# Kernel optimization log

Measured on AMD Instinct MI355X. Metric: run time of the kernel, lower is better.

## Reference

```python
import jax, jax.numpy as jnp
import numpy as np

N_NODES = 50000


def gin_conv(x, src, dst, W, b, eps=0.0):
    # GINConv: nn((1+eps)*x_i + sum_{j in N(i)} x_j)
    agg = jax.ops.segment_sum(x[src], dst, num_segments=N_NODES)  # [N, D]
    h = (1.0 + eps) * x + agg
    return h @ W + b


def setup_inputs() -> dict:
    key = jax.random.key(0)
    ks = jax.random.split(key, 8)
    n, e = N_NODES, 800000
    d_in, d_h, d_out = 128, 128, 64
    feature = jax.random.normal(ks[0], (n, d_in), dtype=jnp.float32)
    edge_index = jax.random.randint(ks[1], (2, e), 0, n, dtype=jnp.int64)
    s1 = 1.0 / np.sqrt(d_in)
    sh = 1.0 / np.sqrt(d_h)
    W1 = jax.random.normal(ks[2], (d_in, d_h), dtype=jnp.float32) * s1
    b1 = jnp.zeros((d_h,), dtype=jnp.float32)
    Wh = jax.random.normal(ks[3], (d_h, d_h), dtype=jnp.float32) * sh
    bh = jnp.zeros((d_h,), dtype=jnp.float32)
    Wo = jax.random.normal(ks[4], (d_h, d_out), dtype=jnp.float32) * sh
    bo = jnp.zeros((d_out,), dtype=jnp.float32)
    return {"feature": feature, "edge_index": edge_index, "W1": W1, "b1": b1,
            "Wh": Wh, "bh": bh, "Wo": Wo, "bo": bo}


def reference(feature, edge_index, W1, b1, Wh, bh, Wo, bo):
    src, dst = edge_index[0], edge_index[1]
    x = gin_conv(feature, src, dst, W1, b1)
    x = jax.nn.relu(x)
    # one hidden layer (layer_num=3); dropout disabled (eval)
    x = gin_conv(x, src, dst, Wh, bh)
    x = jax.nn.relu(x)
    x = gin_conv(x, src, dst, Wo, bo)
    return jax.nn.log_softmax(x, axis=1)
```

## Files before the change

kernel.cpp:

```cpp
#include <hip/hip_runtime.h>

typedef short short8 __attribute__((ext_vector_type(8)));
typedef float f32x4 __attribute__((ext_vector_type(4)));


__device__ inline unsigned short f2bf(float f) {
    union { float f; unsigned u; } v; v.f = f;
    unsigned r = v.u + 0x7fffu + ((v.u >> 16) & 1u);
    return (unsigned short)(r >> 16);
}
__device__ inline unsigned pack2(float a, float b) {
    return (unsigned)f2bf(a) | ((unsigned)f2bf(b) << 16);
}
__device__ inline float bflo(unsigned u) { union { unsigned q; float f; } c; c.q = u << 16; return c.f; }
__device__ inline float bfhi(unsigned u) { union { unsigned q; float f; } c; c.q = u & 0xffff0000u; return c.f; }

#define ACC8(vv)                                     \
    acc[0] += bflo(vv.x); acc[1] += bfhi(vv.x);      \
    acc[2] += bflo(vv.y); acc[3] += bfhi(vv.y);      \
    acc[4] += bflo(vv.z); acc[5] += bfhi(vv.z);      \
    acc[6] += bflo(vv.w); acc[7] += bfhi(vv.w);

template <int TPN, typename F>
__device__ __forceinline__ void gather_acc(float acc[8], const uint4* __restrict__ x,
                                           int lane, int beg, int end, F geti) {
    int k = beg;
    for (; k + 8 <= end; k += 8) {
        int idx[8];
#pragma unroll
        for (int j = 0; j < 8; j++) idx[j] = geti(k + j);
        uint4 v[8];
#pragma unroll
        for (int j = 0; j < 8; j++) v[j] = x[(size_t)idx[j] * TPN + lane];
#pragma unroll
        for (int j = 0; j < 8; j++) { ACC8(v[j]) }
    }
    for (; k + 4 <= end; k += 4) {
        int i0 = geti(k), i1 = geti(k + 1), i2 = geti(k + 2), i3 = geti(k + 3);
        uint4 v0 = x[(size_t)i0 * TPN + lane];
        uint4 v1 = x[(size_t)i1 * TPN + lane];
        uint4 v2 = x[(size_t)i2 * TPN + lane];
        uint4 v3 = x[(size_t)i3 * TPN + lane];
        ACC8(v0) ACC8(v1) ACC8(v2) ACC8(v3)
    }
    for (; k < end; ++k) {
        uint4 v0 = x[(size_t)geti(k) * TPN + lane];
        ACC8(v0)
    }
}


#define EPB 2048
#define NE 8
#define BSH 9
#define MAXBKT 128
#define DCAP 10240

__global__ __launch_bounds__(256) void mega1(const int* __restrict__ dst, int* __restrict__ cnt2d,
                                             int e, int nbkt, int nblk,
                                             const float4* __restrict__ feat, uint2* __restrict__ featb,
                                             int cvtb, int nf4,
                                             const float* __restrict__ W1, const float* __restrict__ Wh,
                                             const float* __restrict__ Wo,
                                             unsigned short* __restrict__ W1t, unsigned short* __restrict__ Wht,
                                             unsigned short* __restrict__ Wot) {
    __shared__ int hist[MAXBKT];
    int t = threadIdx.x, b = blockIdx.x;
    if (b < nblk) {
        for (int j = t; j < nbkt; j += 256) hist[j] = 0;
        __syncthreads();
        int base = b * EPB;
#pragma unroll
        for (int j = 0; j < NE; j++) {
            int idx = base + t + 256 * j;
            if (idx < e) atomicAdd(&hist[dst[idx] >> BSH], 1);
        }
        __syncthreads();
        for (int j = t; j < nbkt; j += 256) cnt2d[j * nblk + b] = hist[j];
    } else if (b < nblk + cvtb) {
        int i = (b - nblk) * 256 + t;
        if (i < nf4) {
            float4 v = feat[i];
            featb[i] = make_uint2(pack2(v.x, v.y), pack2(v.z, v.w));
        }
    } else {
        int i = (b - nblk - cvtb) * 256 + t;
        if (i < 16384) {
            int k = i >> 7, nn = i & 127;
            W1t[nn * 128 + k] = f2bf(W1[i]);
        } else if (i < 32768) {
            int j = i - 16384, k = j >> 7, nn = j & 127;
            Wht[nn * 128 + k] = f2bf(Wh[j]);
        } else if (i < 40960) {
            int j = i - 32768, k = j >> 6, nn = j & 63;
            Wot[nn * 128 + k] = f2bf(Wo[j]);
        }
    }
}

__global__ __launch_bounds__(512) void scanB1(int* __restrict__ cnt2d, int* __restrict__ totals, int nblk) {
    __shared__ int s[512];
    int t = threadIdx.x, b = blockIdx.x;
    int v = (t < nblk) ? cnt2d[b * nblk + t] : 0;
    s[t] = v;
    __syncthreads();
    for (int off = 1; off < 512; off <<= 1) {
        int u = (t >= off) ? s[t - off] : 0;
        __syncthreads();
        s[t] += u;
        __syncthreads();
    }
    if (t < nblk) cnt2d[b * nblk + t] = s[t] - v;
    if (t == nblk - 1) totals[b] = s[t];
}

__global__ __launch_bounds__(128) void scanB2(const int* __restrict__ totals, int* __restrict__ bbase,
                                              int* __restrict__ row_ptr, int nbkt, int n, int e) {
    __shared__ int s[128];
    int t = threadIdx.x;
    int v = (t < nbkt) ? totals[t] : 0;
    s[t] = v;
    __syncthreads();
    for (int off = 1; off < 128; off <<= 1) {
        int u = (t >= off) ? s[t - off] : 0;
        __syncthreads();
        s[t] += u;
        __syncthreads();
    }
    if (t < nbkt) bbase[t] = s[t] - v;
    if (t == 0) row_ptr[n] = e;
}

__global__ __launch_bounds__(256) void binC(const int* __restrict__ src, const int* __restrict__ dst,
                                            const int* __restrict__ cnt2d, const int* __restrict__ bbase,
                                            unsigned* __restrict__ pairs, int e, int nbkt, int nblk) {
    __shared__ int hist[MAXBKT], loff[MAXBKT], cur[MAXBKT], gb[MAXBKT];
    __shared__ int sc[256];
    __shared__ unsigned sorted[EPB];
    int t = threadIdx.x, blk = blockIdx.x;
    for (int b = t; b < nbkt; b += 256) hist[b] = 0;
    __syncthreads();
    int base = blk * EPB;
    int cnt = min(EPB, e - base);
    unsigned packed[NE];
    int bb[NE];
#pragma unroll
    for (int j = 0; j < NE; j++) {
        int idx = base + t + 256 * j;
        bb[j] = -1;
        if (idx < e) {
            unsigned s0 = (unsigned)src[idx], d = (unsigned)dst[idx];
            int b = (int)(d >> BSH);
            bb[j] = b;
            packed[j] = s0 | ((d & ((1u << BSH) - 1)) << 16) | ((unsigned)b << 25);
            atomicAdd(&hist[b], 1);
        }
    }
    __syncthreads();
    int v = (t < nbkt) ? hist[t] : 0;
    sc[t] = v;
    __syncthreads();
    for (int off = 1; off < 256; off <<= 1) {
        int u = (t >= off) ? sc[t - off] : 0;
        __syncthreads();
        sc[t] += u;
        __syncthreads();
    }
    if (t < nbkt) {
        int ex = sc[t] - v;
        loff[t] = ex;
        cur[t] = ex;
        gb[t] = bbase[t] + cnt2d[t * nblk + blk];
    }
    __syncthreads();
#pragma unroll
    for (int j = 0; j < NE; j++) {
        if (bb[j] >= 0) {
            int r = atomicAdd(&cur[bb[j]], 1);
            sorted[r] = packed[j];
        }
    }
    __syncthreads();
    for (int i = t; i < cnt; i += 256) {
        unsigned w = sorted[i];
        int b = (int)(w >> 25);
        pairs[gb[b] + (i - loff[b])] = w;
    }
}

__global__ __launch_bounds__(512) void buildD(const unsigned* __restrict__ pairs,
                                              const int* __restrict__ totals, const int* __restrict__ bbase,
                                              int* __restrict__ row_ptr, unsigned short* __restrict__ csr, int n) {
    __shared__ int hist[512], off[512];
    __shared__ unsigned short lcsr[DCAP];
    int t = threadIdx.x, b = blockIdx.x;
    int cnt = totals[b], base = bbase[b];
    hist[t] = 0;
    __syncthreads();
    for (int i = t; i < cnt; i += 512)
        atomicAdd(&hist[(pairs[base + i] >> 16) & 511], 1);
    __syncthreads();
    int v = hist[t];
    off[t] = v;
    __syncthreads();
    for (int o = 1; o < 512; o <<= 1) {
        int u = (t >= o) ? off[t - o] : 0;
        __syncthreads();
        off[t] += u;
        __syncthreads();
    }
    int excl = off[t] - v;
    int node = (b << BSH) + t;
    if (node < n) row_ptr[node] = base + excl;
    __syncthreads();
    hist[t] = excl;
    __syncthreads();
    for (int i = t; i < cnt; i += 512) {
        unsigned w = pairs[base + i];
        int r = atomicAdd(&hist[(w >> 16) & 511], 1);
        if (r < DCAP) lcsr[r] = (unsigned short)(w & 0xFFFFu);
    }
    __syncthreads();
    int lim = min(cnt, DCAP);
    for (int i = t; i < lim; i += 512) csr[base + i] = lcsr[i];
}


#define ECAP 1024

template <bool SECOND>
__global__ __launch_bounds__(256) void fused_layer(
    const uint4* __restrict__ x, const int* __restrict__ row_ptr,
    const unsigned short* __restrict__ csr,
    const short8* __restrict__ Bt, const float* __restrict__ bias,
    unsigned short* __restrict__ out_h,
    const short8* __restrict__ Bt2,
    unsigned short* __restrict__ out_y,
    int n) {
    __shared__ unsigned short As[16][136];
    __shared__ unsigned short Hs[SECOND ? 16 : 1][SECOND ? 136 : 1];
    __shared__ unsigned short eidx[ECAP];

    int t = threadIdx.x;
    int nl = t >> 4, chunk = t & 15;
    int r0 = blockIdx.x * 16;
    int node = r0 + nl;

    int E0 = row_ptr[r0 < n ? r0 : n];
    int E1 = row_ptr[min(r0 + 16, n)];
    int ecnt = min(E1 - E0, ECAP);
    for (int i = t; i < ecnt; i += 256) eidx[i] = csr[E0 + i];
    __syncthreads();

    float acc[8] = {0.f, 0.f, 0.f, 0.f, 0.f, 0.f, 0.f, 0.f};
    if (node < n) {
        uint4 s0 = x[(size_t)node * 16 + chunk];
        ACC8(s0)
        int beg = row_ptr[node], end = row_ptr[node + 1];
        if (end - E0 <= ECAP) {
            gather_acc<16>(acc, x, chunk, beg - E0, end - E0,
                           [&](int k) { return (int)eidx[k]; });
        } else {
            gather_acc<16>(acc, x, chunk, beg, end,
                           [&](int k) { return (int)csr[k]; });
        }
    }
    uint4 packed;
    packed.x = pack2(acc[0], acc[1]); packed.y = pack2(acc[2], acc[3]);
    packed.z = pack2(acc[4], acc[5]); packed.w = pack2(acc[6], acc[7]);
    ((uint4*)&As[nl][0])[chunk] = packed;
    __syncthreads();

    int wid = t >> 6, lane = t & 63;
    int lm = lane & 15, lq = lane >> 4;

    short8 a[4];
#pragma unroll
    for (int kc = 0; kc < 4; kc++)
        a[kc] = *(const short8*)&As[lm][kc * 32 + lq * 8];

    f32x4 hacc[2];
#pragma unroll
    for (int nt = 0; nt < 2; nt++) hacc[nt] = (f32x4){0.f, 0.f, 0.f, 0.f};
#pragma unroll
    for (int nt = 0; nt < 2; nt++) {
        const short8* Br = Bt + (size_t)((wid * 2 + nt) * 16 + lm) * 16;
#pragma unroll
        for (int kc = 0; kc < 4; kc++)
            hacc[nt] = __builtin_amdgcn_mfma_f32_16x16x32_bf16(a[kc], Br[kc * 4 + lq], hacc[nt], 0, 0, 0);
    }

#pragma unroll
    for (int nt = 0; nt < 2; nt++) {
        int col = (wid * 2 + nt) * 16 + lm;
        float bv = bias[col];
#pragma unroll
        for (int i = 0; i < 4; i++) {
            int row = r0 + lq * 4 + i;
            float v = fmaxf(hacc[nt][i] + bv, 0.f);
            if (SECOND) {
                Hs[lq * 4 + i][col] = f2bf(v);
            } else if (row < n) {
                out_h[(size_t)row * 128 + col] = f2bf(v);
            }
        }
    }

    if (SECOND) {
        __syncthreads();
        short8 a2[4];
#pragma unroll
        for (int kc = 0; kc < 4; kc++)
            a2[kc] = *(const short8*)&Hs[lm][kc * 32 + lq * 8];
        f32x4 yacc = (f32x4){0.f, 0.f, 0.f, 0.f};
        const short8* Br2 = Bt2 + (size_t)(wid * 16 + lm) * 16;
#pragma unroll
        for (int kc = 0; kc < 4; kc++)
            yacc = __builtin_amdgcn_mfma_f32_16x16x32_bf16(a2[kc], Br2[kc * 4 + lq], yacc, 0, 0, 0);
        int col = wid * 16 + lm;
#pragma unroll
        for (int i = 0; i < 4; i++) {
            int row = r0 + lq * 4 + i;
            if (row < n) out_y[(size_t)row * 64 + col] = f2bf(yacc[i]);
        }
    }
}


#define ECAP2 1536

__global__ __launch_bounds__(256) void agg_lsm(
    const uint4* __restrict__ x, float* __restrict__ out,
    const int* __restrict__ row_ptr, const unsigned short* __restrict__ csr,
    const float* __restrict__ bo, int n) {
    __shared__ unsigned short eidx[ECAP2];
    int t = threadIdx.x;
    int r0 = blockIdx.x * 32;
    int node = r0 + (t >> 3), lane = t & 7;

    int E0 = row_ptr[r0 < n ? r0 : n];
    int E1 = row_ptr[min(r0 + 32, n)];
    int ecnt = min(E1 - E0, ECAP2);
    for (int i = t; i < ecnt; i += 256) eidx[i] = csr[E0 + i];
    __syncthreads();

    if (node >= n) return;
    uint4 s0 = x[(size_t)node * 8 + lane];
    float acc[8] = { bflo(s0.x), bfhi(s0.x), bflo(s0.y), bfhi(s0.y),
                     bflo(s0.z), bfhi(s0.z), bflo(s0.w), bfhi(s0.w) };
    int beg = row_ptr[node], end = row_ptr[node + 1];
    if (end - E0 <= ECAP2) {
        gather_acc<8>(acc, x, lane, beg - E0, end - E0,
                      [&](int k) { return (int)eidx[k]; });
    } else {
        gather_acc<8>(acc, x, lane, beg, end,
                      [&](int k) { return (int)csr[k]; });
    }

    const float4* bo4 = (const float4*)bo;
    float4 bA = bo4[lane * 2], bB = bo4[lane * 2 + 1];
    acc[0] += bA.x; acc[1] += bA.y; acc[2] += bA.z; acc[3] += bA.w;
    acc[4] += bB.x; acc[5] += bB.y; acc[6] += bB.z; acc[7] += bB.w;
    float m = acc[0];
#pragma unroll
    for (int j = 1; j < 8; j++) m = fmaxf(m, acc[j]);
#pragma unroll
    for (int off = 1; off < 8; off <<= 1) m = fmaxf(m, __shfl_xor(m, off, 64));
    float s = 0.f;
#pragma unroll
    for (int j = 0; j < 8; j++) s += __expf(acc[j] - m);
#pragma unroll
    for (int off = 1; off < 8; off <<= 1) s += __shfl_xor(s, off, 64);
    float ls = m + __logf(s);
    float4 o0 = make_float4(acc[0] - ls, acc[1] - ls, acc[2] - ls, acc[3] - ls);
    float4 o1 = make_float4(acc[4] - ls, acc[5] - ls, acc[6] - ls, acc[7] - ls);
    float4* op = (float4*)(out + (size_t)node * 64 + lane * 8);
    op[0] = o0;
    op[1] = o1;
}


extern "C" void kernel_launch(void* const* d_in, const int* in_sizes, int n_in,
                              void* d_out, int out_size, void* d_ws, size_t ws_size,
                              hipStream_t stream) {
    const float* feature = (const float*)d_in[0];
    const int*   edges   = (const int*)d_in[1];
    const float* W1 = (const float*)d_in[2];
    const float* b1 = (const float*)d_in[3];
    const float* Wh = (const float*)d_in[4];
    const float* bh = (const float*)d_in[5];
    const float* Wo = (const float*)d_in[6];
    const float* bo = (const float*)d_in[7];

    int n = in_sizes[0] / 128;
    int e = in_sizes[1] / 2;
    const int* src = edges;
    const int* dst = edges + e;

    int nbkt = (n + 511) >> BSH;
    int nblk = (e + EPB - 1) / EPB;
    int nf4 = n * 32;
    int cvtb = (nf4 + 255) / 256;

    char* ws = (char*)d_ws;
    auto take = [&](size_t bytes) {
        char* p = ws;
        ws += (bytes + 255) & ~(size_t)255;
        return p;
    };
    int* cnt2d   = (int*)take((size_t)nbkt * nblk * 4);
    int* totals  = (int*)take((size_t)nbkt * 4);
    int* bbase   = (int*)take((size_t)(nbkt + 1) * 4);
    int* row_ptr = (int*)take((size_t)(n + 1) * 4);
    unsigned* pairs = (unsigned*)take((size_t)e * 4);
    unsigned short* csr = (unsigned short*)take((size_t)e * 2);
    unsigned short* featb = (unsigned short*)take((size_t)n * 128 * 2);
    unsigned short* hb    = (unsigned short*)take((size_t)n * 128 * 2);
    unsigned short* yb    = (unsigned short*)take((size_t)n * 64 * 2);
    unsigned short* W1t = (unsigned short*)take(128 * 128 * 2);
    unsigned short* Wht = (unsigned short*)take(128 * 128 * 2);
    unsigned short* Wot = (unsigned short*)take(64 * 128 * 2);

    mega1<<<nblk + cvtb + 160, 256, 0, stream>>>(
        dst, cnt2d, e, nbkt, nblk,
        (const float4*)feature, (uint2*)featb, cvtb, nf4,
        W1, Wh, Wo, W1t, Wht, Wot);
    scanB1<<<nbkt, 512, 0, stream>>>(cnt2d, totals, nblk);
    scanB2<<<1, 128, 0, stream>>>(totals, bbase, row_ptr, nbkt, n, e);
    binC<<<nblk, 256, 0, stream>>>(src, dst, cnt2d, bbase, pairs, e, nbkt, nblk);
    buildD<<<nbkt, 512, 0, stream>>>(pairs, totals, bbase, row_ptr, csr, n);

    int fblocks = (n + 15) / 16;

    fused_layer<false><<<fblocks, 256, 0, stream>>>(
        (const uint4*)featb, row_ptr, csr, (const short8*)W1t, b1,
        hb, nullptr, nullptr, n);

    fused_layer<true><<<fblocks, 256, 0, stream>>>(
        (const uint4*)hb, row_ptr, csr, (const short8*)Wht, bh,
        nullptr, (const short8*)Wot, yb, n);

    agg_lsm<<<(n + 31) / 32, 256, 0, stream>>>(
        (const uint4*)yb, (float*)d_out, row_ptr, csr, bo, n);
}
```

Measured before the change: 212.2 us.

## Balance edge gather across threads with merge-path split and shared-memory atomics

Replaces the per-node gather, where each thread group walks one node's neighbor list, with an edge-balanced split. Each 16- or 8-thread group takes an equal slice of the block's edges, finds its starting node with a binary search over a shared row-pointer copy, and flushes partial sums into a shared float tile with atomicAdd whenever it crosses a node boundary. This is meant to remove the load imbalance caused by the skewed degree distribution within a block. It costs shared-memory float atomics, a larger fp32 staging tile, and bf16 packing when the MFMA operands are loaded.

After: 310.6 us. 1.46x slower.

```diff
diff --git a/kernel.cpp b/kernel.cpp
--- a/kernel.cpp
+++ b/kernel.cpp
@@ -21,32 +21,48 @@
     acc[4] += bflo(vv.z); acc[5] += bfhi(vv.z);      \
     acc[6] += bflo(vv.w); acc[7] += bfhi(vv.w);
 
-template <int TPN, typename F>
-__device__ __forceinline__ void gather_acc(float acc[8], const uint4* __restrict__ x,
-                                           int lane, int beg, int end, F geti) {
-    int k = beg;
-    for (; k + 8 <= end; k += 8) {
-        int idx[8];
-#pragma unroll
-        for (int j = 0; j < 8; j++) idx[j] = geti(k + j);
+
+template <int PITCH, int TPN, typename F>
+__device__ __forceinline__ void edge_gather(float (*As)[PITCH], const int* __restrict__ rpl,
+                                            const uint4* __restrict__ x, int c,
+                                            int j0, int jend, int nd, F geti) {
+    float acc[8] = {0.f, 0.f, 0.f, 0.f, 0.f, 0.f, 0.f, 0.f};
+    int nxt = rpl[nd + 1];
+    int k = j0;
+    for (; k + 8 <= jend; k += 8) {
         uint4 v[8];
 #pragma unroll
-        for (int j = 0; j < 8; j++) v[j] = x[(size_t)idx[j] * TPN + lane];
-#pragma unroll
-        for (int j = 0; j < 8; j++) { ACC8(v[j]) }
-    }
-    for (; k + 4 <= end; k += 4) {
-        int i0 = geti(k), i1 = geti(k + 1), i2 = geti(k + 2), i3 = geti(k + 3);
-        uint4 v0 = x[(size_t)i0 * TPN + lane];
-        uint4 v1 = x[(size_t)i1 * TPN + lane];
-        uint4 v2 = x[(size_t)i2 * TPN + lane];
-        uint4 v3 = x[(size_t)i3 * TPN + lane];
-        ACC8(v0) ACC8(v1) ACC8(v2) ACC8(v3)
-    }
-    for (; k < end; ++k) {
-        uint4 v0 = x[(size_t)geti(k) * TPN + lane];
+        for (int u = 0; u < 8; u++) v[u] = x[(size_t)geti(k + u) * TPN + c];
+#pragma unroll
+        for (int u = 0; u < 8; u++) {
+            while (k + u >= nxt) {
+#pragma unroll
+                for (int i = 0; i < 8; i++) { atomicAdd(&As[nd][c * 8 + i], acc[i]); acc[i] = 0.f; }
+                ++nd; nxt = rpl[nd + 1];
+            }
+            ACC8(v[u])
+        }
+    }
+    for (; k < jend; ++k) {
+        uint4 v0 = x[(size_t)geti(k) * TPN + c];
+        while (k >= nxt) {
+#pragma unroll
+            for (int i = 0; i < 8; i++) { atomicAdd(&As[nd][c * 8 + i], acc[i]); acc[i] = 0.f; }
+            ++nd; nxt = rpl[nd + 1];
+        }
         ACC8(v0)
     }
+#pragma unroll
+    for (int i = 0; i < 8; i++) atomicAdd(&As[nd][c * 8 + i], acc[i]);
+}
+
+template <int S0>
+__device__ __forceinline__ int ub_search(const int* __restrict__ rpl, int j) {
+    int nd = 0;
+#pragma unroll
+    for (int s = S0; s >= 1; s >>= 1)
+        if (rpl[nd + s] <= j) nd += s;
+    return nd;
 }
 
 
@@ -237,38 +253,49 @@
     const short8* __restrict__ Bt2,
     unsigned short* __restrict__ out_y,
     int n) {
-    __shared__ unsigned short As[16][136];
+    __shared__ float Asf[16][140];
     __shared__ unsigned short Hs[SECOND ? 16 : 1][SECOND ? 136 : 1];
     __shared__ unsigned short eidx[ECAP];
+    __shared__ int rpl[17];
 
     int t = threadIdx.x;
-    int nl = t >> 4, chunk = t & 15;
+    int g = t >> 4, c = t & 15;
     int r0 = blockIdx.x * 16;
-    int node = r0 + nl;
-
-    int E0 = row_ptr[r0 < n ? r0 : n];
+    int node = r0 + g;
+
+    int E0 = row_ptr[r0];
     int E1 = row_ptr[min(r0 + 16, n)];
-    int ecnt = min(E1 - E0, ECAP);
-    for (int i = t; i < ecnt; i += 256) eidx[i] = csr[E0 + i];
-    __syncthreads();
-
-    float acc[8] = {0.f, 0.f, 0.f, 0.f, 0.f, 0.f, 0.f, 0.f};
-    if (node < n) {
-        uint4 s0 = x[(size_t)node * 16 + chunk];
-        ACC8(s0)
-        int beg = row_ptr[node], end = row_ptr[node + 1];
-        if (end - E0 <= ECAP) {
-            gather_acc<16>(acc, x, chunk, beg - E0, end - E0,
-                           [&](int k) { return (int)eidx[k]; });
-        } else {
-            gather_acc<16>(acc, x, chunk, beg, end,
-                           [&](int k) { return (int)csr[k]; });
-        }
-    }
-    uint4 packed;
-    packed.x = pack2(acc[0], acc[1]); packed.y = pack2(acc[2], acc[3]);
-    packed.z = pack2(acc[4], acc[5]); packed.w = pack2(acc[6], acc[7]);
-    ((uint4*)&As[nl][0])[chunk] = packed;
+    int ecnt = E1 - E0;
+    bool fits = (ecnt <= ECAP);
+    int scnt = fits ? ecnt : ECAP;
+    for (int i = t; i < scnt; i += 256) eidx[i] = csr[E0 + i];
+    if (t < 17) rpl[t] = row_ptr[min(r0 + t, n)] - E0;
+
+    {
+        f32x4 lo = {0.f, 0.f, 0.f, 0.f}, hi = {0.f, 0.f, 0.f, 0.f};
+        if (node < n) {
+            uint4 s0 = x[(size_t)node * 16 + c];
+            lo[0] = bflo(s0.x); lo[1] = bfhi(s0.x); lo[2] = bflo(s0.y); lo[3] = bfhi(s0.y);
+            hi[0] = bflo(s0.z); hi[1] = bfhi(s0.z); hi[2] = bflo(s0.w); hi[3] = bfhi(s0.w);
+        }
+        *(f32x4*)&Asf[g][c * 8] = lo;
+        *(f32x4*)&Asf[g][c * 8 + 4] = hi;
+    }
+    __syncthreads();
+
+    {
+        int L = (ecnt + 15) >> 4;
+        int j0 = g * L, jend = min(j0 + L, ecnt);
+        if (j0 < jend) {
+            int nd = ub_search<8>(rpl, j0);
+            if (fits)
+                edge_gather<140, 16>(Asf, rpl, x, c, j0, jend, nd,
+                                     [&](int k) { return (int)eidx[k]; });
+            else
+                edge_gather<140, 16>(Asf, rpl, x, c, j0, jend, nd,
+                                     [&](int k) { return (int)csr[E0 + k]; });
+        }
+    }
     __syncthreads();
 
     int wid = t >> 6, lane = t & 63;
@@ -276,8 +303,14 @@
 
     short8 a[4];
 #pragma unroll
-    for (int kc = 0; kc < 4; kc++)
-        a[kc] = *(const short8*)&As[lm][kc * 32 + lq * 8];
+    for (int kc = 0; kc < 4; kc++) {
+        const f32x4* Ar = (const f32x4*)&Asf[lm][kc * 32 + lq * 8];
+        f32x4 lo = Ar[0], hi = Ar[1];
+        uint4 up;
+        up.x = pack2(lo[0], lo[1]); up.y = pack2(lo[2], lo[3]);
+        up.z = pack2(hi[0], hi[1]); up.w = pack2(hi[2], hi[3]);
+        a[kc] = *(short8*)&up;
+    }
 
     f32x4 hacc[2];
 #pragma unroll
@@ -333,32 +366,58 @@
     const uint4* __restrict__ x, float* __restrict__ out,
     const int* __restrict__ row_ptr, const unsigned short* __restrict__ csr,
     const float* __restrict__ bo, int n) {
+    __shared__ float Asf[32][72];
     __shared__ unsigned short eidx[ECAP2];
+    __shared__ int rpl[33];
+
     int t = threadIdx.x;
+    int g = t >> 3, c = t & 7;
     int r0 = blockIdx.x * 32;
-    int node = r0 + (t >> 3), lane = t & 7;
-
-    int E0 = row_ptr[r0 < n ? r0 : n];
+    int node = r0 + g;
+
+    int E0 = row_ptr[r0];
     int E1 = row_ptr[min(r0 + 32, n)];
-    int ecnt = min(E1 - E0, ECAP2);
-    for (int i = t; i < ecnt; i += 256) eidx[i] = csr[E0 + i];
+    int ecnt = E1 - E0;
+    bool fits = (ecnt <= ECAP2);
+    int scnt = fits ? ecnt : ECAP2;
+    for (int i = t; i < scnt; i += 256) eidx[i] = csr[E0 + i];
+    if (t < 33) rpl[t] = row_ptr[min(r0 + t, n)] - E0;
+
+    {
+        f32x4 lo = {0.f, 0.f, 0.f, 0.f}, hi = {0.f, 0.f, 0.f, 0.f};
+        if (node < n) {
+            uint4 s0 = x[(size_t)node * 8 + c];
+            lo[0] = bflo(s0.x); lo[1] = bfhi(s0.x); lo[2] = bflo(s0.y); lo[3] = bfhi(s0.y);
+            hi[0] = bflo(s0.z); hi[1] = bfhi(s0.z); hi[2] = bflo(s0.w); hi[3] = bfhi(s0.w);
+        }
+        *(f32x4*)&Asf[g][c * 8] = lo;
+        *(f32x4*)&Asf[g][c * 8 + 4] = hi;
+    }
+    __syncthreads();
+
+    {
+        int L = (ecnt + 31) >> 5;
+        int j0 = g * L, jend = min(j0 + L, ecnt);
+        if (j0 < jend) {
+            int nd = ub_search<16>(rpl, j0);
+            if (fits)
+                edge_gather<72, 8>(Asf, rpl, x, c, j0, jend, nd,
+                                   [&](int k) { return (int)eidx[k]; });
+            else
+                edge_gather<72, 8>(Asf, rpl, x, c, j0, jend, nd,
+                                   [&](int k) { return (int)csr[E0 + k]; });
+        }
+    }
     __syncthreads();
 
     if (node >= n) return;
-    uint4 s0 = x[(size_t)node * 8 + lane];
-    float acc[8] = { bflo(s0.x), bfhi(s0.x), bflo(s0.y), bfhi(s0.y),
-                     bflo(s0.z), bfhi(s0.z), bflo(s0.w), bfhi(s0.w) };
-    int beg = row_ptr[node], end = row_ptr[node + 1];
-    if (end - E0 <= ECAP2) {
-        gather_acc<8>(acc, x, lane, beg - E0, end - E0,
-                      [&](int k) { return (int)eidx[k]; });
-    } else {
-        gather_acc<8>(acc, x, lane, beg, end,
-                      [&](int k) { return (int)csr[k]; });
-    }
+
+    const f32x4* Ar = (const f32x4*)&Asf[g][c * 8];
+    f32x4 aLo = Ar[0], aHi = Ar[1];
+    float acc[8] = {aLo[0], aLo[1], aLo[2], aLo[3], aHi[0], aHi[1], aHi[2], aHi[3]};
 
     const float4* bo4 = (const float4*)bo;
-    float4 bA = bo4[lane * 2], bB = bo4[lane * 2 + 1];
+    float4 bA = bo4[c * 2], bB = bo4[c * 2 + 1];
     acc[0] += bA.x; acc[1] += bA.y; acc[2] += bA.z; acc[3] += bA.w;
     acc[4] += bB.x; acc[5] += bB.y; acc[6] += bB.z; acc[7] += bB.w;
     float m = acc[0];
@@ -374,7 +433,7 @@
     float ls = m + __logf(s);
     float4 o0 = make_float4(acc[0] - ls, acc[1] - ls, acc[2] - ls, acc[3] - ls);
     float4 o1 = make_float4(acc[4] - ls, acc[5] - ls, acc[6] - ls, acc[7] - ls);
-    float4* op = (float4*)(out + (size_t)node * 64 + lane * 8);
+    float4* op = (float4*)(out + (size_t)node * 64 + c * 8);
     op[0] = o0;
     op[1] = o1;
 }
```
